# Kernel optimization log

Measured on AMD Instinct MI355X. Metric: run time of the kernel, lower is better.

## Reference

```python
import jax, jax.numpy as jnp
import numpy as np

D_MODEL = 384
HEAD_SIZE = 64
CONTEXT = 100


def setup_inputs() -> dict:
    key = jax.random.key(0)
    kx, kq, kk, kv = jax.random.split(key, 4)
    x = jax.random.normal(kx, (1024, CONTEXT, D_MODEL), dtype=jnp.float32)
    s = 1.0 / np.sqrt(D_MODEL)
    Wq = jax.random.normal(kq, (D_MODEL, HEAD_SIZE), dtype=jnp.float32) * s
    Wk = jax.random.normal(kk, (D_MODEL, HEAD_SIZE), dtype=jnp.float32) * s
    Wv = jax.random.normal(kv, (D_MODEL, HEAD_SIZE), dtype=jnp.float32) * s
    return {"x": x, "Wq": Wq, "Wk": Wk, "Wv": Wv}


def reference(x, Wq, Wk, Wv):
    B, T, C = x.shape
    q = jnp.einsum('btc,ch->bth', x, Wq)
    k = jnp.einsum('btc,ch->bth', x, Wk)
    v = jnp.einsum('btc,ch->bth', x, Wv)
    # Faithful to source bug: divide by d**(-0.5) == multiply by sqrt(d)
    scale = jnp.asarray(k.shape[-1], x.dtype) ** 0.5
    wei = jnp.einsum('bth,bsh->bts', q, k) * scale  # [B,T,T]
    causal = jnp.tril(jnp.ones((T, T), dtype=bool))
    wei = jnp.where(causal, wei, -jnp.inf)
    wei = jax.nn.softmax(wei, axis=-1)
    # dropout: eval mode (identity)
    return jnp.einsum('bts,bsh->bth', wei, v)
```

## Files before the change

kernel.cpp:

```cpp
#include <hip/hip_runtime.h>
#include <hip/hip_fp16.h>

#define T_CTX 100
#define C_DIM 384
#define H_DIM 64

typedef _Float16 half8   __attribute__((ext_vector_type(8)));
typedef _Float16 half4_t __attribute__((ext_vector_type(4)));
typedef _Float16 half2_t __attribute__((ext_vector_type(2)));
typedef float    f32x4   __attribute__((ext_vector_type(4)));

#define QH_OFF 0
#define QL_OFF 7168
#define KH_OFF 14336
#define KL_OFF 21504
#define VT_OFF 28672
#define PS_OFF 0
#define SMEM_BYTES 73728

__global__ void prep_w_kernel(const float* __restrict__ Wq,
                              const float* __restrict__ Wk,
                              const float* __restrict__ Wv,
                              _Float16* __restrict__ wf_hi,
                              _Float16* __restrict__ wf_lo) {
    int idx = blockIdx.x * 256 + threadIdx.x;
    if (idx >= 9216) return;
    int lane  = idx & 63;
    int chunk = (idx >> 6) % 12;
    int jt    = idx / (64 * 12);
    int col   = jt * 16 + (lane & 15);
    const float* W = (col < 64) ? Wq : ((col < 128) ? Wk : Wv);
    int h = col & 63;
    int cbase = chunk * 32 + (lane >> 4) * 8;
    #pragma unroll
    for (int e = 0; e < 8; ++e) {
        float f = W[(size_t)(cbase + e) * H_DIM + h];
        _Float16 hi = (_Float16)f;
        _Float16 lo = (_Float16)(f - (float)hi);
        size_t o = (size_t)idx * 8 + e;
        wf_hi[o] = hi;
        wf_lo[o] = lo;
    }
}

__device__ inline void cvt4(f32x4 v, half4_t& hh, half4_t& ll) {
    #pragma unroll
    for (int u = 0; u < 4; ++u) {
        _Float16 h = (_Float16)v[u];
        hh[u] = h;
        ll[u] = (_Float16)(v[u] - (float)h);
    }
}

__device__ inline int qk_off(int row, int h) {
    int LANE = (row & 15) + ((h >> 3) & 3) * 16;
    int LS   = (LANE ^ (LANE >> 2)) & 63;
    return (row >> 4) * 1024 + ((h >> 5) & 1) * 512 + LS * 8 + (h & 7);
}

__global__ __launch_bounds__(512, 4)
void head_kernel(const float* __restrict__ x,
                 const _Float16* __restrict__ wf_hi,
                 const _Float16* __restrict__ wf_lo,
                 float* __restrict__ out) {
    extern __shared__ _Float16 sm[];

    const int b    = blockIdx.x;
    const int tid  = threadIdx.x;
    const int lane = tid & 63;
    const int wid  = tid >> 6;
    const int l15  = lane & 15;
    const int lg   = lane >> 4;
    const int mh   = wid >> 2;
    const int nw   = wid & 3;
    const int NI   = (mh == 0) ? 4 : 3;
    const bool isK = (nw >= 2);
    const int swl8 = ((lane ^ (lane >> 2)) & 63) * 8;

    int t0, t1;
    const _Float16 *pw0, *pw1, *pw2, *pw3;
    if (!isK) {
        t0 = nw * 2; t1 = t0 + 1;
        pw0 = wf_hi + (size_t)t0 * 6144;
        pw1 = wf_hi + (size_t)t1 * 6144;
        pw2 = wf_hi + (size_t)(8 + nw * 2) * 6144;
        pw3 = wf_hi + (size_t)(9 + nw * 2) * 6144;
    } else {
        t0 = 4 + (nw - 2) * 2; t1 = t0 + 1;
        pw0 = wf_hi + (size_t)t0 * 6144;
        pw1 = wf_hi + (size_t)t1 * 6144;
        pw2 = wf_lo + (size_t)t0 * 6144;
        pw3 = wf_lo + (size_t)t1 * 6144;
    }

    const float* xb = x + (size_t)b * T_CTX * C_DIM;

    f32x4 acc0[4], acc1[4], acc2[4], acc3[4];
    #pragma unroll
    for (int i = 0; i < 4; ++i) {
        acc0[i] = (f32x4){0.f,0.f,0.f,0.f};
        acc1[i] = (f32x4){0.f,0.f,0.f,0.f};
        acc2[i] = (f32x4){0.f,0.f,0.f,0.f};
        acc3[i] = (f32x4){0.f,0.f,0.f,0.f};
    }

    #pragma unroll
    for (int s = 0; s < 2; ++s) {
        int f4  = tid + s * 512;
        int row = f4 >> 3;
        int c4  = f4 & 7;
        f32x4 v = (f32x4){0.f, 0.f, 0.f, 0.f};
        if (row < T_CTX) v = *(const f32x4*)(xb + (size_t)row * C_DIM + c4 * 4);
        half4_t hh, ll;
        cvt4(v, hh, ll);
        int o = row * 40 + c4 * 4;
        *(half4_t*)(sm + o)        = hh;
        *(half4_t*)(sm + 5120 + o) = ll;
    }
    half8 W0 = *(const half8*)(pw0 + lane * 8);
    half8 W1 = *(const half8*)(pw1 + lane * 8);
    half8 W2 = *(const half8*)(pw2 + lane * 8);
    half8 W3 = *(const half8*)(pw3 + lane * 8);
    __syncthreads();

    #pragma unroll 1
    for (int kc = 0; kc < 12; ++kc) {
        const int nk = kc + 1;
        f32x4 ld[2];
        half8 N0 = W0, N1 = W1, N2 = W2, N3 = W3;
        if (nk < 12) {
            #pragma unroll
            for (int s = 0; s < 2; ++s) {
                int f4  = tid + s * 512;
                int row = f4 >> 3;
                int c4  = f4 & 7;
                ld[s] = (f32x4){0.f, 0.f, 0.f, 0.f};
                if (row < T_CTX)
                    ld[s] = *(const f32x4*)(xb + (size_t)row * C_DIM + nk * 32 + c4 * 4);
            }
            const int wo = nk * 512 + lane * 8;
            N0 = *(const half8*)(pw0 + wo);
            N1 = *(const half8*)(pw1 + wo);
            N2 = *(const half8*)(pw2 + wo);
            N3 = *(const half8*)(pw3 + wo);
        }

        const _Float16* xh = sm + (kc & 1) * 10240;
        const _Float16* xl = xh + 5120;
        #pragma unroll
        for (int i = 0; i < 4; ++i) {
            if (i >= NI) break;
            int row = mh * 64 + i * 16 + l15;
            int o = row * 40 + lg * 8;
            half8 ah = *(const half8*)(xh + o);
            half8 al = *(const half8*)(xl + o);
            acc0[i] = __builtin_amdgcn_mfma_f32_16x16x32_f16(ah, W0, acc0[i], 0, 0, 0);
            acc0[i] = __builtin_amdgcn_mfma_f32_16x16x32_f16(al, W0, acc0[i], 0, 0, 0);
            acc1[i] = __builtin_amdgcn_mfma_f32_16x16x32_f16(ah, W1, acc1[i], 0, 0, 0);
            acc1[i] = __builtin_amdgcn_mfma_f32_16x16x32_f16(al, W1, acc1[i], 0, 0, 0);
            if (!isK) {
                acc2[i] = __builtin_amdgcn_mfma_f32_16x16x32_f16(ah, W2, acc2[i], 0, 0, 0);
                acc3[i] = __builtin_amdgcn_mfma_f32_16x16x32_f16(ah, W3, acc3[i], 0, 0, 0);
            } else {
                acc0[i] = __builtin_amdgcn_mfma_f32_16x16x32_f16(ah, W2, acc0[i], 0, 0, 0);
                acc1[i] = __builtin_amdgcn_mfma_f32_16x16x32_f16(ah, W3, acc1[i], 0, 0, 0);
            }
        }

        if (nk < 12) {
            const int nb = (nk & 1) * 10240;
            #pragma unroll
            for (int s = 0; s < 2; ++s) {
                int f4  = tid + s * 512;
                int row = f4 >> 3;
                int c4  = f4 & 7;
                half4_t hh, ll;
                cvt4(ld[s], hh, ll);
                int o = row * 40 + c4 * 4;
                *(half4_t*)(sm + nb + o)        = hh;
                *(half4_t*)(sm + nb + 5120 + o) = ll;
            }
        }
        __syncthreads();
        W0 = N0; W1 = N1; W2 = N2; W3 = N3;
    }

    {
        int jh = tid >> 7;
        int w2 = (tid & 127) * 2;
        *(half2_t*)(sm + VT_OFF + jh * 2048 + 1792 + w2) =
            (half2_t){(_Float16)0.f, (_Float16)0.f};
    }

    #pragma unroll
    for (int i = 0; i < 4; ++i) {
        if (i >= NI) break;
        #pragma unroll
        for (int r = 0; r < 4; ++r) {
            int row = mh * 64 + i * 16 + lg * 4 + r;
            if (!isK) {
                {
                    int h = t0 * 16 + l15;
                    int off = qk_off(row, h);
                    float v0 = acc0[i][r];
                    _Float16 hh = (_Float16)v0;
                    sm[QH_OFF + off] = hh;
                    sm[QL_OFF + off] = (_Float16)(v0 - (float)hh);
                }
                {
                    int h = t1 * 16 + l15;
                    int off = qk_off(row, h);
                    float v0 = acc1[i][r];
                    _Float16 hh = (_Float16)v0;
                    sm[QH_OFF + off] = hh;
                    sm[QL_OFF + off] = (_Float16)(v0 - (float)hh);
                }
                {
                    int h = nw * 32 + l15;
                    int off = (h >> 4) * 2048 + (row >> 5) * 512
                            + (((row >> 3) & 3) * 16 + (h & 15)) * 8 + (row & 7);
                    sm[VT_OFF + off] = (_Float16)acc2[i][r];
                }
                {
                    int h = nw * 32 + 16 + l15;
                    int off = (h >> 4) * 2048 + (row >> 5) * 512
                            + (((row >> 3) & 3) * 16 + (h & 15)) * 8 + (row & 7);
                    sm[VT_OFF + off] = (_Float16)acc3[i][r];
                }
            } else {
                {
                    int h = (t0 - 4) * 16 + l15;
                    int off = qk_off(row, h);
                    float v0 = acc0[i][r];
                    _Float16 hh = (_Float16)v0;
                    sm[KH_OFF + off] = hh;
                    sm[KL_OFF + off] = (_Float16)(v0 - (float)hh);
                }
                {
                    int h = (t1 - 4) * 16 + l15;
                    int off = qk_off(row, h);
                    float v0 = acc1[i][r];
                    _Float16 hh = (_Float16)v0;
                    sm[KH_OFF + off] = hh;
                    sm[KL_OFF + off] = (_Float16)(v0 - (float)hh);
                }
            }
        }
    }
    __syncthreads();

    f32x4 sacc[7];
    float rsum[4] = {0.f, 0.f, 0.f, 0.f};
    const float SC = 8.0f * 1.44269504088896f;

    if (wid < 7) {
        #pragma unroll
        for (int j = 0; j < 7; ++j) sacc[j] = (f32x4){0.f,0.f,0.f,0.f};
        #pragma unroll
        for (int kk = 0; kk < 2; ++kk) {
            half8 qh = *(const half8*)(sm + QH_OFF + wid * 1024 + kk * 512 + swl8);
            half8 ql = *(const half8*)(sm + QL_OFF + wid * 1024 + kk * 512 + swl8);
            #pragma unroll
            for (int j = 0; j < 7; ++j) {
                half8 kh = *(const half8*)(sm + KH_OFF + j * 1024 + kk * 512 + swl8);
                half8 kl = *(const half8*)(sm + KL_OFF + j * 1024 + kk * 512 + swl8);
                sacc[j] = __builtin_amdgcn_mfma_f32_16x16x32_f16(qh, kh, sacc[j], 0, 0, 0);
                sacc[j] = __builtin_amdgcn_mfma_f32_16x16x32_f16(ql, kh, sacc[j], 0, 0, 0);
                sacc[j] = __builtin_amdgcn_mfma_f32_16x16x32_f16(qh, kl, sacc[j], 0, 0, 0);
            }
        }
        float rmax[4] = {-1e30f, -1e30f, -1e30f, -1e30f};
        #pragma unroll
        for (int j = 0; j < 7; ++j) {
            int key = j * 16 + l15;
            #pragma unroll
            for (int r = 0; r < 4; ++r) {
                int row = wid * 16 + lg * 4 + r;
                float s = (key <= row && key < T_CTX) ? sacc[j][r] * SC : -1e30f;
                sacc[j][r] = s;
                rmax[r] = fmaxf(rmax[r], s);
            }
        }
        #pragma unroll
        for (int r = 0; r < 4; ++r) {
            #pragma unroll
            for (int d = 1; d < 16; d <<= 1)
                rmax[r] = fmaxf(rmax[r], __shfl_xor(rmax[r], d, 64));
            rsum[r] = rmax[r];
        }
    }
    __syncthreads();

    if (wid < 7) {
        float rmax[4];
        #pragma unroll
        for (int r = 0; r < 4; ++r) { rmax[r] = rsum[r]; rsum[r] = 0.f; }
        #pragma unroll
        for (int j = 0; j < 7; ++j) {
            int key = j * 16 + l15;
            #pragma unroll
            for (int r = 0; r < 4; ++r) {
                float p = exp2f(sacc[j][r] - rmax[r]);
                rsum[r] += p;
                int a = lg * 4 + r;
                int LANE = ((key >> 3) & 3) * 16 + a;
                int LS = (LANE ^ (LANE >> 2)) & 63;
                int off = wid * 2048 + (key >> 5) * 512 + LS * 8 + (key & 7);
                sm[PS_OFF + off] = (_Float16)p;
            }
        }
        #pragma unroll
        for (int r = 0; r < 4; ++r) {
            int key = 112 + l15;
            int a = lg * 4 + r;
            int LANE = ((key >> 3) & 3) * 16 + a;
            int LS = (LANE ^ (LANE >> 2)) & 63;
            int off = wid * 2048 + (key >> 5) * 512 + LS * 8 + (key & 7);
            sm[PS_OFF + off] = (_Float16)0.f;
            #pragma unroll
            for (int d = 1; d < 16; d <<= 1)
                rsum[r] += __shfl_xor(rsum[r], d, 64);
        }
    }
    __syncthreads();

    if (wid < 7) {
        f32x4 oacc[4];
        #pragma unroll
        for (int j = 0; j < 4; ++j) oacc[j] = (f32x4){0.f,0.f,0.f,0.f};
        #pragma unroll
        for (int kk = 0; kk < 4; ++kk) {
            half8 pa = *(const half8*)(sm + PS_OFF + wid * 2048 + kk * 512 + swl8);
            #pragma unroll
            for (int jh = 0; jh < 4; ++jh) {
                half8 vb = *(const half8*)(sm + VT_OFF + jh * 2048 + kk * 512 + lane * 8);
                oacc[jh] = __builtin_amdgcn_mfma_f32_16x16x32_f16(pa, vb, oacc[jh], 0, 0, 0);
            }
        }
        float rinv[4];
        #pragma unroll
        for (int r = 0; r < 4; ++r) rinv[r] = 1.0f / rsum[r];
        #pragma unroll
        for (int jh = 0; jh < 4; ++jh) {
            #pragma unroll
            for (int r = 0; r < 4; ++r) {
                int t = wid * 16 + lg * 4 + r;
                if (t < T_CTX)
                    out[((size_t)b * T_CTX + t) * H_DIM + jh * 16 + l15] = oacc[jh][r] * rinv[r];
            }
        }
    }
}

extern "C" void kernel_launch(void* const* d_in, const int* in_sizes, int n_in,
                              void* d_out, int out_size, void* d_ws, size_t ws_size,
                              hipStream_t stream) {
    const float* x  = (const float*)d_in[0];
    const float* Wq = (const float*)d_in[1];
    const float* Wk = (const float*)d_in[2];
    const float* Wv = (const float*)d_in[3];

    _Float16* wf_hi = (_Float16*)d_ws;
    _Float16* wf_lo = wf_hi + (size_t)9216 * 8;

    prep_w_kernel<<<36, 256, 0, stream>>>(Wq, Wk, Wv, wf_hi, wf_lo);

    (void)hipFuncSetAttribute((const void*)head_kernel,
                              hipFuncAttributeMaxDynamicSharedMemorySize, SMEM_BYTES);
    head_kernel<<<1024, 512, SMEM_BYTES, stream>>>(x, wf_hi, wf_lo, (float*)d_out);
}
```

Measured before the change: 66.75 us.

## Skip causally masked tiles in attention and drop LDS XOR swizzle

```diff
diff --git a/kernel.cpp b/kernel.cpp
--- a/kernel.cpp
+++ b/kernel.cpp
@@ -53,9 +53,8 @@
 }
 
 __device__ inline int qk_off(int row, int h) {
-    int LANE = (row & 15) + ((h >> 3) & 3) * 16;
-    int LS   = (LANE ^ (LANE >> 2)) & 63;
-    return (row >> 4) * 1024 + ((h >> 5) & 1) * 512 + LS * 8 + (h & 7);
+    return (row >> 4) * 1024 + ((h >> 5) & 1) * 512
+         + (((h >> 3) & 3) * 16 + (row & 15)) * 8 + (h & 7);
 }
 
 __global__ __launch_bounds__(512, 4)
@@ -75,7 +74,7 @@
     const int nw   = wid & 3;
     const int NI   = (mh == 0) ? 4 : 3;
     const bool isK = (nw >= 2);
-    const int swl8 = ((lane ^ (lane >> 2)) & 63) * 8;
+    const int ln8  = lane * 8;
 
     int t0, t1;
     const _Float16 *pw0, *pw1, *pw2, *pw3;
@@ -117,10 +116,10 @@
         *(half4_t*)(sm + o)        = hh;
         *(half4_t*)(sm + 5120 + o) = ll;
     }
-    half8 W0 = *(const half8*)(pw0 + lane * 8);
-    half8 W1 = *(const half8*)(pw1 + lane * 8);
-    half8 W2 = *(const half8*)(pw2 + lane * 8);
-    half8 W3 = *(const half8*)(pw3 + lane * 8);
+    half8 W0 = *(const half8*)(pw0 + ln8);
+    half8 W1 = *(const half8*)(pw1 + ln8);
+    half8 W2 = *(const half8*)(pw2 + ln8);
+    half8 W3 = *(const half8*)(pw3 + ln8);
     __syncthreads();
 
     #pragma unroll 1
@@ -138,7 +137,7 @@
                 if (row < T_CTX)
                     ld[s] = *(const f32x4*)(xb + (size_t)row * C_DIM + nk * 32 + c4 * 4);
             }
-            const int wo = nk * 512 + lane * 8;
+            const int wo = nk * 512 + ln8;
             N0 = *(const half8*)(pw0 + wo);
             N1 = *(const half8*)(pw1 + wo);
             N2 = *(const half8*)(pw2 + wo);
@@ -258,12 +257,13 @@
         for (int j = 0; j < 7; ++j) sacc[j] = (f32x4){0.f,0.f,0.f,0.f};
         #pragma unroll
         for (int kk = 0; kk < 2; ++kk) {
-            half8 qh = *(const half8*)(sm + QH_OFF + wid * 1024 + kk * 512 + swl8);
-            half8 ql = *(const half8*)(sm + QL_OFF + wid * 1024 + kk * 512 + swl8);
+            half8 qh = *(const half8*)(sm + QH_OFF + wid * 1024 + kk * 512 + ln8);
+            half8 ql = *(const half8*)(sm + QL_OFF + wid * 1024 + kk * 512 + ln8);
             #pragma unroll
             for (int j = 0; j < 7; ++j) {
-                half8 kh = *(const half8*)(sm + KH_OFF + j * 1024 + kk * 512 + swl8);
-                half8 kl = *(const half8*)(sm + KL_OFF + j * 1024 + kk * 512 + swl8);
+                if (j > wid) break;
+                half8 kh = *(const half8*)(sm + KH_OFF + j * 1024 + kk * 512 + ln8);
+                half8 kl = *(const half8*)(sm + KL_OFF + j * 1024 + kk * 512 + ln8);
                 sacc[j] = __builtin_amdgcn_mfma_f32_16x16x32_f16(qh, kh, sacc[j], 0, 0, 0);
                 sacc[j] = __builtin_amdgcn_mfma_f32_16x16x32_f16(ql, kh, sacc[j], 0, 0, 0);
                 sacc[j] = __builtin_amdgcn_mfma_f32_16x16x32_f16(qh, kl, sacc[j], 0, 0, 0);
@@ -272,6 +272,7 @@
         float rmax[4] = {-1e30f, -1e30f, -1e30f, -1e30f};
         #pragma unroll
         for (int j = 0; j < 7; ++j) {
+            if (j > wid) break;
             int key = j * 16 + l15;
             #pragma unroll
             for (int r = 0; r < 4; ++r) {
@@ -297,26 +298,30 @@
         for (int r = 0; r < 4; ++r) { rmax[r] = rsum[r]; rsum[r] = 0.f; }
         #pragma unroll
         for (int j = 0; j < 7; ++j) {
+            if (j > wid) break;
             int key = j * 16 + l15;
             #pragma unroll
             for (int r = 0; r < 4; ++r) {
                 float p = exp2f(sacc[j][r] - rmax[r]);
                 rsum[r] += p;
                 int a = lg * 4 + r;
-                int LANE = ((key >> 3) & 3) * 16 + a;
-                int LS = (LANE ^ (LANE >> 2)) & 63;
-                int off = wid * 2048 + (key >> 5) * 512 + LS * 8 + (key & 7);
+                int off = wid * 2048 + (key >> 5) * 512
+                        + (((key >> 3) & 3) * 16 + a) * 8 + (key & 7);
                 sm[PS_OFF + off] = (_Float16)p;
             }
         }
+        if ((wid & 1) == 0) {
+            int key = (wid + 1) * 16 + l15;
+            #pragma unroll
+            for (int r = 0; r < 4; ++r) {
+                int a = lg * 4 + r;
+                int off = wid * 2048 + (key >> 5) * 512
+                        + (((key >> 3) & 3) * 16 + a) * 8 + (key & 7);
+                sm[PS_OFF + off] = (_Float16)0.f;
+            }
+        }
         #pragma unroll
         for (int r = 0; r < 4; ++r) {
-            int key = 112 + l15;
-            int a = lg * 4 + r;
-            int LANE = ((key >> 3) & 3) * 16 + a;
-            int LS = (LANE ^ (LANE >> 2)) & 63;
-            int off = wid * 2048 + (key >> 5) * 512 + LS * 8 + (key & 7);
-            sm[PS_OFF + off] = (_Float16)0.f;
             #pragma unroll
             for (int d = 1; d < 16; d <<= 1)
                 rsum[r] += __shfl_xor(rsum[r], d, 64);
@@ -328,12 +333,14 @@
         f32x4 oacc[4];
         #pragma unroll
         for (int j = 0; j < 4; ++j) oacc[j] = (f32x4){0.f,0.f,0.f,0.f};
+        const int kkmax = wid >> 1;
         #pragma unroll
         for (int kk = 0; kk < 4; ++kk) {
-            half8 pa = *(const half8*)(sm + PS_OFF + wid * 2048 + kk * 512 + swl8);
+            if (kk > kkmax) break;
+            half8 pa = *(const half8*)(sm + PS_OFF + wid * 2048 + kk * 512 + ln8);
             #pragma unroll
             for (int jh = 0; jh < 4; ++jh) {
-                half8 vb = *(const half8*)(sm + VT_OFF + jh * 2048 + kk * 512 + lane * 8);
+                half8 vb = *(const half8*)(sm + VT_OFF + jh * 2048 + kk * 512 + ln8);
                 oacc[jh] = __builtin_amdgcn_mfma_f32_16x16x32_f16(pa, vb, oacc[jh], 0, 0, 0);
             }
         }
```

New measurement: 64.97 us. 2.7% less time.
